# Kernel tuning notes

Hardware: AMD Instinct MI355X
Metric: run time of the kernel (lower is better)

The kernel has to match this reference:

```python
import jax, jax.numpy as jnp
import numpy as np

B, N, DIM = 4, 2048, 512
HEADS, DIM_HEAD = 8, 64
INNER = HEADS * DIM_HEAD  # == DIM, so to_out is Identity
LN_EPS = 1e-5
MASK_FILL = 1e-8  # faithful to torch.where(mask, attn, 1e-08)


def setup_inputs() -> dict:
    key = jax.random.key(0)
    k1, k2 = jax.random.split(key)
    x = jax.random.normal(k1, (B, N, DIM), dtype=jnp.float32)
    gamma = jnp.ones((DIM,), dtype=jnp.float32)
    beta = jnp.zeros((DIM,), dtype=jnp.float32)
    w_qkv = jax.random.normal(k2, (3 * INNER, DIM), dtype=jnp.float32) * (DIM ** -0.5)
    mask = jnp.tril(jnp.ones((N, N), dtype=bool))  # causal boolean mask, asserted 2-D in source
    return {"x": x, "gamma": gamma, "beta": beta, "w_qkv": w_qkv, "mask": mask}


def reference(x, gamma, beta, w_qkv, mask):
    # LayerNorm over last dim
    mu = jnp.mean(x, axis=-1, keepdims=True)
    var = jnp.var(x, axis=-1, keepdims=True)
    h = (x - mu) * jax.lax.rsqrt(var + LN_EPS) * gamma + beta
    # qkv projection (no bias), chunk into q, k, v
    qkv = h @ w_qkv.T  # [B, N, 3*INNER]
    q, k, v = jnp.split(qkv, 3, axis=-1)

    def to_heads(t):  # b n (h d) -> b h n d
        return t.reshape(B, N, HEADS, DIM_HEAD).transpose(0, 2, 1, 3)

    q, k, v = to_heads(q), to_heads(k), to_heads(v)
    # NOTE: original forward does NOT apply self.scale
    attn = jnp.einsum('bhnd,bhmd->bhnm', q, k)
    attn = jnp.where(mask[None, None, :, :], attn, MASK_FILL)
    p = jax.nn.softmax(attn, axis=-1)
    out = jnp.einsum('bhnm,bhmd->bhnd', p, v)
    out = out.transpose(0, 2, 1, 3).reshape(B, N, INNER)  # b h n d -> b n (h d)
    return out  # to_out is Identity since INNER == DIM
```

## Files before the change

kernel.cpp:

```cpp
#include <hip/hip_runtime.h>
#include <hip/hip_bf16.h>
#include <math.h>

#define B_  4
#define N_  2048
#define DIM_ 512
#define HEADS_ 8
#define QKV_ 1536
#define MASK_C 1e-8f
#define M_FIX 12.0f
#define LOG2E 1.44269504f

typedef __bf16 bf16_t;
typedef bf16_t bf16x8 __attribute__((ext_vector_type(8)));
typedef float  f32x4  __attribute__((ext_vector_type(4)));

__device__ __forceinline__ bf16_t f2b(float x) { return (bf16_t)x; }
__device__ __forceinline__ float  b2f(bf16_t x) { return (float)x; }

__device__ __forceinline__ f32x4 mfma16(bf16x8 a, bf16x8 b, f32x4 c) {
    return __builtin_amdgcn_mfma_f32_16x16x32_bf16(a, b, c, 0, 0, 0);
}

__device__ __forceinline__ void gload16(const bf16_t* g, bf16_t* l) {
    __builtin_amdgcn_global_load_lds(
        (const __attribute__((address_space(1))) unsigned int*)g,
        (__attribute__((address_space(3))) unsigned int*)l, 16, 0, 0);
}

__global__ __launch_bounds__(256) void ln_wsplit_kernel(const float* __restrict__ x,
                                                        const float* __restrict__ gamma,
                                                        const float* __restrict__ beta,
                                                        bf16_t* __restrict__ hh,
                                                        bf16_t* __restrict__ hl,
                                                        const float* __restrict__ wq,
                                                        bf16_t* __restrict__ wh,
                                                        bf16_t* __restrict__ wl) {
    int blk = blockIdx.x;
    int t = threadIdx.x;
    if (blk >= B_ * N_) {
        int i = ((blk - B_ * N_) * 256 + t) * 4;
        float4 v = *(const float4*)&wq[i];
        float vv[4] = {v.x, v.y, v.z, v.w};
        #pragma unroll
        for (int j = 0; j < 4; j++) {
            bf16_t hi = f2b(vv[j]);
            wh[i + j] = hi;
            wl[i + j] = f2b(vv[j] - b2f(hi));
        }
        return;
    }
    int row = blk;
    const float* xr = x + (size_t)row * DIM_;
    float e0 = xr[t];
    float e1 = xr[t + 256];
    float s  = e0 + e1;
    float sq = e0 * e0 + e1 * e1;
    for (int off = 32; off; off >>= 1) {
        s  += __shfl_xor(s, off);
        sq += __shfl_xor(sq, off);
    }
    __shared__ float red[8];
    int w = t >> 6;
    if ((t & 63) == 0) { red[w] = s; red[4 + w] = sq; }
    __syncthreads();
    float S  = red[0] + red[1] + red[2] + red[3];
    float SQ = red[4] + red[5] + red[6] + red[7];
    float mu = S * (1.0f / DIM_);
    float var = SQ * (1.0f / DIM_) - mu * mu;
    float rs = rsqrtf(var + 1e-5f);
    float y0 = (e0 - mu) * rs * gamma[t] + beta[t];
    float y1 = (e1 - mu) * rs * gamma[t + 256] + beta[t + 256];
    size_t base = (size_t)row * DIM_;
    bf16_t h0 = f2b(y0), h1 = f2b(y1);
    hh[base + t] = h0;       hl[base + t] = f2b(y0 - b2f(h0));
    hh[base + t + 256] = h1; hl[base + t + 256] = f2b(y1 - b2f(h1));
}

__global__ __launch_bounds__(256, 3) void qkv_gemm(const bf16_t* __restrict__ hh,
                                                   const bf16_t* __restrict__ hl,
                                                   const bf16_t* __restrict__ wh,
                                                   const bf16_t* __restrict__ wl,
                                                   bf16_t* __restrict__ qh, bf16_t* __restrict__ ql,
                                                   bf16_t* __restrict__ kh, bf16_t* __restrict__ kl,
                                                   bf16_t* __restrict__ vth,
                                                   float* __restrict__ part) {
    __shared__ __align__(16) bf16_t smem[16896];
    bf16_t* Ah = smem;
    bf16_t* Al = smem + 4096;
    bf16_t* Bh = smem + 8192;
    bf16_t* Bl = smem + 12288;
    int bm = blockIdx.x & 63;
    int bn = blockIdx.x >> 6;
    int t = threadIdx.x;
    int w = t >> 6, lane = t & 63, quad = lane >> 4, l16 = lane & 15;

    f32x4 acc[2][8];
    #pragma unroll
    for (int i = 0; i < 2; i++)
        #pragma unroll
        for (int j = 0; j < 8; j++) acc[i][j] = (f32x4)(0.0f);

    int sl = lane & 15, sg = lane >> 4;
    size_t gA0 = (size_t)(bm * 128 + w * 32 + sl) * 512 + sg * 8;
    size_t gB0 = (size_t)(bn * 128 + w * 32 + sl) * 512 + sg * 8;

    for (int k0 = 0; k0 < 512; k0 += 32) {
        __syncthreads();
        #pragma unroll
        for (int c = 0; c < 2; c++) {
            size_t ga = gA0 + k0 + (size_t)c * 16 * 512;
            size_t gb = gB0 + k0 + (size_t)c * 16 * 512;
            int lo = w * 1024 + c * 512;
            gload16(&hh[ga], Ah + lo);
            gload16(&hl[ga], Al + lo);
            gload16(&wh[gb], Bh + lo);
            gload16(&wl[gb], Bl + lo);
        }
        __syncthreads();

        bf16x8 aH[2], aL[2];
        #pragma unroll
        for (int mt = 0; mt < 2; mt++) {
            int ab = (w * 2 + mt) * 512 + quad * 128 + l16 * 8;
            aH[mt] = *(const bf16x8*)&Ah[ab];
            aL[mt] = *(const bf16x8*)&Al[ab];
        }
        #pragma unroll
        for (int nt = 0; nt < 8; nt++) {
            int bb = nt * 512 + quad * 128 + l16 * 8;
            bf16x8 bH = *(const bf16x8*)&Bh[bb];
            bf16x8 bL = *(const bf16x8*)&Bl[bb];
            #pragma unroll
            for (int mt = 0; mt < 2; mt++) {
                acc[mt][nt] = mfma16(aH[mt], bH, acc[mt][nt]);
                acc[mt][nt] = mfma16(aH[mt], bL, acc[mt][nt]);
                acc[mt][nt] = mfma16(aL[mt], bH, acc[mt][nt]);
            }
        }
    }

    if (bn < 8) {
        #pragma unroll
        for (int mt = 0; mt < 2; mt++)
            #pragma unroll
            for (int nt = 0; nt < 8; nt++)
                #pragma unroll
                for (int reg = 0; reg < 4; reg++) {
                    float v = acc[mt][nt][reg];
                    int row = bm * 128 + w * 32 + mt * 16 + quad * 4 + reg;
                    int n = bn * 128 + nt * 16 + l16;
                    bf16_t hi = f2b(v);
                    bf16_t lo = f2b(v - b2f(hi));
                    if (n < 512) {
                        size_t a = (size_t)row * 512 + n;
                        qh[a] = hi; ql[a] = lo;
                    } else {
                        size_t a = (size_t)row * 512 + (n - 512);
                        kh[a] = hi; kl[a] = lo;
                    }
                }
    } else {
        int bb = bm >> 4, key0 = (bm & 15) * 128;
        int n = t & 127, mc = (t >> 7) * 64;
        int head = (bn - 8) * 2 + (n >> 6), dd = n & 63;
        size_t obase = ((size_t)((bb * 8 + head) * 64 + dd)) * 2048 + key0 + mc;
        float Ssum = 0.0f;
        #pragma unroll
        for (int pass = 0; pass < 2; pass++) {
            __syncthreads();
            #pragma unroll
            for (int mt = 0; mt < 2; mt++)
                #pragma unroll
                for (int nt = 0; nt < 8; nt++)
                    #pragma unroll
                    for (int reg = 0; reg < 4; reg++) {
                        float v = acc[mt][nt][reg];
                        bf16_t hi = f2b(v);
                        bf16_t val = pass ? f2b(v - b2f(hi)) : hi;
                        smem[(w * 32 + mt * 16 + quad * 4 + reg) * 132 + nt * 16 + l16] = val;
                    }
            __syncthreads();
            #pragma unroll
            for (int i = 0; i < 64; i += 8) {
                __align__(16) bf16_t v8[8];
                #pragma unroll
                for (int j = 0; j < 8; j++) {
                    v8[j] = smem[(mc + i + j) * 132 + n];
                    Ssum += b2f(v8[j]);
                }
                if (pass == 0)
                    *(uint4*)&vth[obase + i] = *(const uint4*)v8;
            }
        }
        int tt = (key0 >> 6) + (mc >> 6);
        part[((size_t)((bb * 8 + head) * 32 + tt)) * 64 + dd] = Ssum;
    }
}

__global__ __launch_bounds__(256, 4) void attn_kernel(const bf16_t* __restrict__ qh,
                                                      const bf16_t* __restrict__ ql,
                                                      const bf16_t* __restrict__ kh,
                                                      const bf16_t* __restrict__ kl,
                                                      const bf16_t* __restrict__ vth,
                                                      const float* __restrict__ part,
                                                      float* __restrict__ out) {
    __shared__ __align__(16) bf16_t smem[17152];
    __shared__ float sufl[4][64];
    char* lds = (char*)smem;
    bf16_t* Ps = smem + 12288;

    int blk = blockIdx.x;
    int bh = blk & 31;
    int gi = blk >> 5;
    int g3 = gi & 7;
    int q4 = gi >> 3;
    int rt;
    if (q4 == 0)      rt = 31 - g3;
    else if (q4 == 1) rt = g3;
    else if (q4 == 2) rt = 23 - g3;
    else              rt = 8 + g3;
    int b = bh >> 3, head = bh & 7;
    int t = threadIdx.x;
    int w = t >> 6, lane = t & 63, quad = lane >> 4, l16 = lane & 15;

    {
        int d = t & 63, g = t >> 6;
        float s = 0.0f;
        for (int tt = rt + 1 + g; tt < 32; tt += 4)
            s += part[((size_t)bh * 32 + tt) * 64 + d];
        sufl[g][d] = s;
    }

    bf16x8 qAH[2], qAL[2];
    {
        int qrow = rt * 64 + w * 16 + l16;
        size_t g = ((size_t)(b * N_ + qrow)) * 512 + head * 64 + quad * 8;
        qAH[0] = *(const bf16x8*)&qh[g];
        qAH[1] = *(const bf16x8*)&qh[g + 32];
        qAL[0] = *(const bf16x8*)&ql[g];
        qAL[1] = *(const bf16x8*)&ql[g + 32];
    }
    bf16x8 ones;
    #pragma unroll
    for (int j = 0; j < 8; j++) ones[j] = f2b(1.0f);

    f32x4 O[4];
    #pragma unroll
    for (int nt = 0; nt < 4; nt++) O[nt] = (f32x4)(0.0f);
    f32x4 Lacc = (f32x4)(0.0f);
    const float mbias = M_FIX * LOG2E;

    int r = t >> 2, c16 = t & 3;
    int swz = (r & 7) << 4;
    int lk0 = r * 128 + ((c16 * 32)      ^ swz);
    int lk1 = r * 128 + ((c16 * 32 + 16) ^ swz);
    size_t gk = ((size_t)(b * N_ + r)) * 512 + head * 64 + c16 * 16;
    size_t gv = ((size_t)(bh * 64 + r)) * 2048 + c16 * 16;

    uint4 pKh0 = *(const uint4*)&kh[gk];
    uint4 pKh1 = *(const uint4*)&kh[gk + 8];
    uint4 pKl0 = *(const uint4*)&kl[gk];
    uint4 pKl1 = *(const uint4*)&kl[gk + 8];
    uint4 pVh0 = *(const uint4*)&vth[gv];
    uint4 pVh1 = *(const uint4*)&vth[gv + 8];

    for (int jt = 0; jt <= rt; jt++) {
        __syncthreads();
        *(uint4*)(lds + lk0)         = pKh0;
        *(uint4*)(lds + lk1)         = pKh1;
        *(uint4*)(lds + 8192 + lk0)  = pKl0;
        *(uint4*)(lds + 8192 + lk1)  = pKl1;
        *(uint4*)(lds + 16384 + lk0) = pVh0;
        *(uint4*)(lds + 16384 + lk1) = pVh1;
        __syncthreads();

        if (jt < rt) {
            gk += (size_t)64 * 512;
            gv += 64;
            pKh0 = *(const uint4*)&kh[gk];
            pKh1 = *(const uint4*)&kh[gk + 8];
            pKl0 = *(const uint4*)&kl[gk];
            pKl1 = *(const uint4*)&kl[gk + 8];
            pVh0 = *(const uint4*)&vth[gv];
            pVh1 = *(const uint4*)&vth[gv + 8];
        }

        f32x4 S[4];
        #pragma unroll
        for (int nt = 0; nt < 4; nt++) S[nt] = (f32x4)(0.0f);
        __builtin_amdgcn_s_setprio(1);
        #pragma unroll
        for (int khf = 0; khf < 2; khf++) {
            #pragma unroll
            for (int nt = 0; nt < 4; nt++) {
                int row = nt * 16 + l16;
                int bc = (khf * 64 + quad * 16) ^ ((row & 7) << 4);
                bf16x8 bH = *(const bf16x8*)(lds + row * 128 + bc);
                bf16x8 bL = *(const bf16x8*)(lds + 8192 + row * 128 + bc);
                S[nt] = mfma16(qAH[khf], bH, S[nt]);
                S[nt] = mfma16(qAH[khf], bL, S[nt]);
                S[nt] = mfma16(qAL[khf], bH, S[nt]);
            }
        }
        __builtin_amdgcn_s_setprio(0);

        if (jt == rt) {
            int lrow = w * 16 + quad * 4;
            #pragma unroll
            for (int nt = 0; nt < 4; nt++)
                #pragma unroll
                for (int reg = 0; reg < 4; reg++)
                    if (nt * 16 + l16 > lrow + reg) S[nt][reg] = MASK_C;
        }

        #pragma unroll
        for (int nt = 0; nt < 4; nt++)
            #pragma unroll
            for (int reg = 0; reg < 4; reg++)
                Ps[(w * 16 + quad * 4 + reg) * 76 + nt * 16 + l16] =
                    f2b(exp2f(fmaf(S[nt][reg], LOG2E, -mbias)));

        bf16x8 pH[2];
        #pragma unroll
        for (int khf = 0; khf < 2; khf++)
            pH[khf] = *(const bf16x8*)&Ps[(w * 16 + l16) * 76 + khf * 32 + quad * 8];

        __builtin_amdgcn_s_setprio(1);
        #pragma unroll
        for (int khf = 0; khf < 2; khf++) Lacc = mfma16(pH[khf], ones, Lacc);

        #pragma unroll
        for (int khf = 0; khf < 2; khf++) {
            #pragma unroll
            for (int nt = 0; nt < 4; nt++) {
                int row = nt * 16 + l16;
                int bc = (khf * 64 + quad * 16) ^ ((row & 7) << 4);
                bf16x8 vB = *(const bf16x8*)(lds + 16384 + row * 128 + bc);
                O[nt] = mfma16(pH[khf], vB, O[nt]);
            }
        }
        __builtin_amdgcn_s_setprio(0);
    }

    float L[4];
    #pragma unroll
    for (int reg = 0; reg < 4; reg++) L[reg] = Lacc[reg];
    int cnt = N_ - (rt + 1) * 64;
    if (cnt > 0) {
        float pc = expf(MASK_C - M_FIX);
        float sv[4];
        #pragma unroll
        for (int nt = 0; nt < 4; nt++) {
            int d = nt * 16 + l16;
            sv[nt] = sufl[0][d] + sufl[1][d] + sufl[2][d] + sufl[3][d];
        }
        #pragma unroll
        for (int reg = 0; reg < 4; reg++) {
            L[reg] += pc * (float)cnt;
            #pragma unroll
            for (int nt = 0; nt < 4; nt++) O[nt][reg] += pc * sv[nt];
        }
    }

    #pragma unroll
    for (int reg = 0; reg < 4; reg++) {
        float rl = 1.0f / L[reg];
        int row = rt * 64 + w * 16 + quad * 4 + reg;
        #pragma unroll
        for (int nt = 0; nt < 4; nt++)
            out[((size_t)(b * N_ + row)) * DIM_ + head * 64 + nt * 16 + l16] =
                O[nt][reg] * rl;
    }
}

extern "C" void kernel_launch(void* const* d_in, const int* in_sizes, int n_in,
                              void* d_out, int out_size, void* d_ws, size_t ws_size,
                              hipStream_t stream) {
    const float* x     = (const float*)d_in[0];
    const float* gamma = (const float*)d_in[1];
    const float* beta  = (const float*)d_in[2];
    const float* w_qkv = (const float*)d_in[3];
    float* out = (float*)d_out;

    const size_t HW = (size_t)8192 * 512;
    const size_t WN = (size_t)1536 * 512;
    bf16_t* hh  = (bf16_t*)d_ws;
    bf16_t* hl  = hh + HW;
    bf16_t* qh  = hl + HW;
    bf16_t* ql  = qh + HW;
    bf16_t* kh  = ql + HW;
    bf16_t* kl  = kh + HW;
    bf16_t* vth = kl + HW;
    bf16_t* vtl = vth + HW;
    bf16_t* wh  = vtl + HW;
    bf16_t* wl  = wh + WN;
    float*  part = (float*)(wl + WN);

    ln_wsplit_kernel<<<B_ * N_ + 768, 256, 0, stream>>>(x, gamma, beta, hh, hl,
                                                        w_qkv, wh, wl);
    qkv_gemm<<<768, 256, 0, stream>>>(hh, hl, wh, wl, qh, ql, kh, kl, vth, part);
    attn_kernel<<<1024, 256, 0, stream>>>(qh, ql, kh, kl, vth, part, out);
}
```

Before: 207.1 us.

## Stage QKV GEMM through registers and read attention K/V directly from global

The QKV GEMM replaces direct global-to-LDS loads with register-prefetched tiles written into a padded (stride 40) LDS layout, overlapping the next k-slice fetch with compute. The attention kernel drops LDS staging of K/V entirely and has each wave load its MFMA operands straight from global memory (relying on L1/L2), removing two block barriers per tile. This trades sync and LDS traffic for redundant global loads across the four waves and exposed load latency without explicit prefetch.

```diff
diff --git a/kernel.cpp b/kernel.cpp
--- a/kernel.cpp
+++ b/kernel.cpp
@@ -20,12 +20,6 @@
 
 __device__ __forceinline__ f32x4 mfma16(bf16x8 a, bf16x8 b, f32x4 c) {
     return __builtin_amdgcn_mfma_f32_16x16x32_bf16(a, b, c, 0, 0, 0);
-}
-
-__device__ __forceinline__ void gload16(const bf16_t* g, bf16_t* l) {
-    __builtin_amdgcn_global_load_lds(
-        (const __attribute__((address_space(1))) unsigned int*)g,
-        (__attribute__((address_space(3))) unsigned int*)l, 16, 0, 0);
 }
 
 __global__ __launch_bounds__(256) void ln_wsplit_kernel(const float* __restrict__ x,
@@ -85,11 +79,11 @@
                                                    bf16_t* __restrict__ kh, bf16_t* __restrict__ kl,
                                                    bf16_t* __restrict__ vth,
                                                    float* __restrict__ part) {
-    __shared__ __align__(16) bf16_t smem[16896];
+    __shared__ __align__(16) bf16_t smem[20480];
     bf16_t* Ah = smem;
-    bf16_t* Al = smem + 4096;
-    bf16_t* Bh = smem + 8192;
-    bf16_t* Bl = smem + 12288;
+    bf16_t* Al = smem + 5120;
+    bf16_t* Bh = smem + 10240;
+    bf16_t* Bl = smem + 15360;
     int bm = blockIdx.x & 63;
     int bn = blockIdx.x >> 6;
     int t = threadIdx.x;
@@ -101,36 +95,53 @@
         #pragma unroll
         for (int j = 0; j < 8; j++) acc[i][j] = (f32x4)(0.0f);
 
-    int sl = lane & 15, sg = lane >> 4;
-    size_t gA0 = (size_t)(bm * 128 + w * 32 + sl) * 512 + sg * 8;
-    size_t gB0 = (size_t)(bn * 128 + w * 32 + sl) * 512 + sg * 8;
+    int sr = t >> 1, skc = (t & 1) * 16;
+    size_t gA = (size_t)(bm * 128 + sr) * 512 + skc;
+    size_t gB = (size_t)(bn * 128 + sr) * 512 + skc;
+
+    uint4 rAh0 = *(const uint4*)&hh[gA];
+    uint4 rAh1 = *(const uint4*)&hh[gA + 8];
+    uint4 rAl0 = *(const uint4*)&hl[gA];
+    uint4 rAl1 = *(const uint4*)&hl[gA + 8];
+    uint4 rBh0 = *(const uint4*)&wh[gB];
+    uint4 rBh1 = *(const uint4*)&wh[gB + 8];
+    uint4 rBl0 = *(const uint4*)&wl[gB];
+    uint4 rBl1 = *(const uint4*)&wl[gB + 8];
 
     for (int k0 = 0; k0 < 512; k0 += 32) {
         __syncthreads();
-        #pragma unroll
-        for (int c = 0; c < 2; c++) {
-            size_t ga = gA0 + k0 + (size_t)c * 16 * 512;
-            size_t gb = gB0 + k0 + (size_t)c * 16 * 512;
-            int lo = w * 1024 + c * 512;
-            gload16(&hh[ga], Ah + lo);
-            gload16(&hl[ga], Al + lo);
-            gload16(&wh[gb], Bh + lo);
-            gload16(&wl[gb], Bl + lo);
-        }
+        *(uint4*)&Ah[sr * 40 + skc]     = rAh0;
+        *(uint4*)&Ah[sr * 40 + skc + 8] = rAh1;
+        *(uint4*)&Al[sr * 40 + skc]     = rAl0;
+        *(uint4*)&Al[sr * 40 + skc + 8] = rAl1;
+        *(uint4*)&Bh[sr * 40 + skc]     = rBh0;
+        *(uint4*)&Bh[sr * 40 + skc + 8] = rBh1;
+        *(uint4*)&Bl[sr * 40 + skc]     = rBl0;
+        *(uint4*)&Bl[sr * 40 + skc + 8] = rBl1;
         __syncthreads();
 
+        if (k0 < 480) {
+            int kn = k0 + 32;
+            rAh0 = *(const uint4*)&hh[gA + kn];
+            rAh1 = *(const uint4*)&hh[gA + kn + 8];
+            rAl0 = *(const uint4*)&hl[gA + kn];
+            rAl1 = *(const uint4*)&hl[gA + kn + 8];
+            rBh0 = *(const uint4*)&wh[gB + kn];
+            rBh1 = *(const uint4*)&wh[gB + kn + 8];
+            rBl0 = *(const uint4*)&wl[gB + kn];
+            rBl1 = *(const uint4*)&wl[gB + kn + 8];
+        }
+
         bf16x8 aH[2], aL[2];
         #pragma unroll
         for (int mt = 0; mt < 2; mt++) {
-            int ab = (w * 2 + mt) * 512 + quad * 128 + l16 * 8;
-            aH[mt] = *(const bf16x8*)&Ah[ab];
-            aL[mt] = *(const bf16x8*)&Al[ab];
+            aH[mt] = *(const bf16x8*)&Ah[(w * 32 + mt * 16 + l16) * 40 + quad * 8];
+            aL[mt] = *(const bf16x8*)&Al[(w * 32 + mt * 16 + l16) * 40 + quad * 8];
         }
         #pragma unroll
         for (int nt = 0; nt < 8; nt++) {
-            int bb = nt * 512 + quad * 128 + l16 * 8;
-            bf16x8 bH = *(const bf16x8*)&Bh[bb];
-            bf16x8 bL = *(const bf16x8*)&Bl[bb];
+            bf16x8 bH = *(const bf16x8*)&Bh[(nt * 16 + l16) * 40 + quad * 8];
+            bf16x8 bL = *(const bf16x8*)&Bl[(nt * 16 + l16) * 40 + quad * 8];
             #pragma unroll
             for (int mt = 0; mt < 2; mt++) {
                 acc[mt][nt] = mfma16(aH[mt], bH, acc[mt][nt]);
@@ -205,10 +216,8 @@
                                                       const bf16_t* __restrict__ vth,
                                                       const float* __restrict__ part,
                                                       float* __restrict__ out) {
-    __shared__ __align__(16) bf16_t smem[17152];
+    __shared__ __align__(16) bf16_t Ps[4][16][76];
     __shared__ float sufl[4][64];
-    char* lds = (char*)smem;
-    bf16_t* Ps = smem + 12288;
 
     int blk = blockIdx.x;
     int bh = blk & 31;
@@ -225,11 +234,11 @@
     int w = t >> 6, lane = t & 63, quad = lane >> 4, l16 = lane & 15;
 
     {
-        int d = t & 63, g = t >> 6;
+        int d = t & 63;
         float s = 0.0f;
-        for (int tt = rt + 1 + g; tt < 32; tt += 4)
+        for (int tt = rt + 1 + w; tt < 32; tt += 4)
             s += part[((size_t)bh * 32 + tt) * 64 + d];
-        sufl[g][d] = s;
+        sufl[w][d] = s;
     }
 
     bf16x8 qAH[2], qAL[2];
@@ -251,40 +260,12 @@
     f32x4 Lacc = (f32x4)(0.0f);
     const float mbias = M_FIX * LOG2E;
 
-    int r = t >> 2, c16 = t & 3;
-    int swz = (r & 7) << 4;
-    int lk0 = r * 128 + ((c16 * 32)      ^ swz);
-    int lk1 = r * 128 + ((c16 * 32 + 16) ^ swz);
-    size_t gk = ((size_t)(b * N_ + r)) * 512 + head * 64 + c16 * 16;
-    size_t gv = ((size_t)(bh * 64 + r)) * 2048 + c16 * 16;
-
-    uint4 pKh0 = *(const uint4*)&kh[gk];
-    uint4 pKh1 = *(const uint4*)&kh[gk + 8];
-    uint4 pKl0 = *(const uint4*)&kl[gk];
-    uint4 pKl1 = *(const uint4*)&kl[gk + 8];
-    uint4 pVh0 = *(const uint4*)&vth[gv];
-    uint4 pVh1 = *(const uint4*)&vth[gv + 8];
+    const bf16_t* kHb = kh + ((size_t)(b * N_ + l16)) * 512 + head * 64 + quad * 8;
+    const bf16_t* kLb = kl + ((size_t)(b * N_ + l16)) * 512 + head * 64 + quad * 8;
+    const bf16_t* vBb = vth + ((size_t)(bh * 64 + l16)) * 2048 + quad * 8;
 
     for (int jt = 0; jt <= rt; jt++) {
-        __syncthreads();
-        *(uint4*)(lds + lk0)         = pKh0;
-        *(uint4*)(lds + lk1)         = pKh1;
-        *(uint4*)(lds + 8192 + lk0)  = pKl0;
-        *(uint4*)(lds + 8192 + lk1)  = pKl1;
-        *(uint4*)(lds + 16384 + lk0) = pVh0;
-        *(uint4*)(lds + 16384 + lk1) = pVh1;
-        __syncthreads();
-
-        if (jt < rt) {
-            gk += (size_t)64 * 512;
-            gv += 64;
-            pKh0 = *(const uint4*)&kh[gk];
-            pKh1 = *(const uint4*)&kh[gk + 8];
-            pKl0 = *(const uint4*)&kl[gk];
-            pKl1 = *(const uint4*)&kl[gk + 8];
-            pVh0 = *(const uint4*)&vth[gv];
-            pVh1 = *(const uint4*)&vth[gv + 8];
-        }
+        size_t krow = (size_t)jt * 64 * 512;
 
         f32x4 S[4];
         #pragma unroll
@@ -294,10 +275,9 @@
         for (int khf = 0; khf < 2; khf++) {
             #pragma unroll
             for (int nt = 0; nt < 4; nt++) {
-                int row = nt * 16 + l16;
-                int bc = (khf * 64 + quad * 16) ^ ((row & 7) << 4);
-                bf16x8 bH = *(const bf16x8*)(lds + row * 128 + bc);
-                bf16x8 bL = *(const bf16x8*)(lds + 8192 + row * 128 + bc);
+                size_t a = krow + (size_t)(nt * 16) * 512 + khf * 32;
+                bf16x8 bH = *(const bf16x8*)(kHb + a);
+                bf16x8 bL = *(const bf16x8*)(kLb + a);
                 S[nt] = mfma16(qAH[khf], bH, S[nt]);
                 S[nt] = mfma16(qAH[khf], bL, S[nt]);
                 S[nt] = mfma16(qAL[khf], bH, S[nt]);
@@ -305,6 +285,14 @@
         }
         __builtin_amdgcn_s_setprio(0);
 
+        bf16x8 vB[2][4];
+        #pragma unroll
+        for (int khf = 0; khf < 2; khf++)
+            #pragma unroll
+            for (int nt = 0; nt < 4; nt++)
+                vB[khf][nt] = *(const bf16x8*)(vBb + (size_t)(nt * 16) * 2048 +
+                                               jt * 64 + khf * 32);
+
         if (jt == rt) {
             int lrow = w * 16 + quad * 4;
             #pragma unroll
@@ -318,30 +306,27 @@
         for (int nt = 0; nt < 4; nt++)
             #pragma unroll
             for (int reg = 0; reg < 4; reg++)
-                Ps[(w * 16 + quad * 4 + reg) * 76 + nt * 16 + l16] =
+                Ps[w][quad * 4 + reg][nt * 16 + l16] =
                     f2b(exp2f(fmaf(S[nt][reg], LOG2E, -mbias)));
 
         bf16x8 pH[2];
         #pragma unroll
         for (int khf = 0; khf < 2; khf++)
-            pH[khf] = *(const bf16x8*)&Ps[(w * 16 + l16) * 76 + khf * 32 + quad * 8];
+            pH[khf] = *(const bf16x8*)&Ps[w][l16][khf * 32 + quad * 8];
 
         __builtin_amdgcn_s_setprio(1);
         #pragma unroll
         for (int khf = 0; khf < 2; khf++) Lacc = mfma16(pH[khf], ones, Lacc);
 
         #pragma unroll
-        for (int khf = 0; khf < 2; khf++) {
-            #pragma unroll
-            for (int nt = 0; nt < 4; nt++) {
-                int row = nt * 16 + l16;
-                int bc = (khf * 64 + quad * 16) ^ ((row & 7) << 4);
-                bf16x8 vB = *(const bf16x8*)(lds + 16384 + row * 128 + bc);
-                O[nt] = mfma16(pH[khf], vB, O[nt]);
-            }
-        }
+        for (int khf = 0; khf < 2; khf++)
+            #pragma unroll
+            for (int nt = 0; nt < 4; nt++)
+                O[nt] = mfma16(pH[khf], vB[khf][nt], O[nt]);
         __builtin_amdgcn_s_setprio(0);
     }
+
+    __syncthreads();
 
     float L[4];
     #pragma unroll
```

New measurement: 309.3 us. 49.3% more time.

## Register-prefetch QKV GEMM tiles into padded LDS instead of direct global-to-LDS loads

Applied to the files above, without the earlier changes.

The QKV GEMM stops using global_load_lds for its tiles. It now prefetches the next K-slice into registers while the current slice computes, then writes it to an LDS layout padded to a row stride of 40 to avoid bank conflicts. The LayerNorm kernel switches to float2 loads and packed 4-byte bf16 stores. The aim is to overlap global latency with MFMA work, at the cost of more VGPRs and LDS, which may lower occupancy under launch_bounds(256,3).

```diff
diff --git a/kernel.cpp b/kernel.cpp
--- a/kernel.cpp
+++ b/kernel.cpp
@@ -20,12 +20,6 @@
 
 __device__ __forceinline__ f32x4 mfma16(bf16x8 a, bf16x8 b, f32x4 c) {
     return __builtin_amdgcn_mfma_f32_16x16x32_bf16(a, b, c, 0, 0, 0);
-}
-
-__device__ __forceinline__ void gload16(const bf16_t* g, bf16_t* l) {
-    __builtin_amdgcn_global_load_lds(
-        (const __attribute__((address_space(1))) unsigned int*)g,
-        (__attribute__((address_space(3))) unsigned int*)l, 16, 0, 0);
 }
 
 __global__ __launch_bounds__(256) void ln_wsplit_kernel(const float* __restrict__ x,
@@ -52,8 +46,8 @@
     }
     int row = blk;
     const float* xr = x + (size_t)row * DIM_;
-    float e0 = xr[t];
-    float e1 = xr[t + 256];
+    float2 xv = *(const float2*)&xr[2 * t];
+    float e0 = xv.x, e1 = xv.y;
     float s  = e0 + e1;
     float sq = e0 * e0 + e1 * e1;
     for (int off = 32; off; off >>= 1) {
@@ -69,12 +63,16 @@
     float mu = S * (1.0f / DIM_);
     float var = SQ * (1.0f / DIM_) - mu * mu;
     float rs = rsqrtf(var + 1e-5f);
-    float y0 = (e0 - mu) * rs * gamma[t] + beta[t];
-    float y1 = (e1 - mu) * rs * gamma[t + 256] + beta[t + 256];
-    size_t base = (size_t)row * DIM_;
+    float2 gv = *(const float2*)&gamma[2 * t];
+    float2 bv = *(const float2*)&beta[2 * t];
+    float y0 = (e0 - mu) * rs * gv.x + bv.x;
+    float y1 = (e1 - mu) * rs * gv.y + bv.y;
+    size_t base = (size_t)row * DIM_ + 2 * t;
     bf16_t h0 = f2b(y0), h1 = f2b(y1);
-    hh[base + t] = h0;       hl[base + t] = f2b(y0 - b2f(h0));
-    hh[base + t + 256] = h1; hl[base + t + 256] = f2b(y1 - b2f(h1));
+    __align__(4) bf16_t hp[2] = {h0, h1};
+    __align__(4) bf16_t lp[2] = {f2b(y0 - b2f(h0)), f2b(y1 - b2f(h1))};
+    *(unsigned int*)&hh[base] = *(unsigned int*)hp;
+    *(unsigned int*)&hl[base] = *(unsigned int*)lp;
 }
 
 __global__ __launch_bounds__(256, 3) void qkv_gemm(const bf16_t* __restrict__ hh,
@@ -85,11 +83,11 @@
                                                    bf16_t* __restrict__ kh, bf16_t* __restrict__ kl,
                                                    bf16_t* __restrict__ vth,
                                                    float* __restrict__ part) {
-    __shared__ __align__(16) bf16_t smem[16896];
+    __shared__ __align__(16) bf16_t smem[20480];
     bf16_t* Ah = smem;
-    bf16_t* Al = smem + 4096;
-    bf16_t* Bh = smem + 8192;
-    bf16_t* Bl = smem + 12288;
+    bf16_t* Al = smem + 5120;
+    bf16_t* Bh = smem + 10240;
+    bf16_t* Bl = smem + 15360;
     int bm = blockIdx.x & 63;
     int bn = blockIdx.x >> 6;
     int t = threadIdx.x;
@@ -101,36 +99,53 @@
         #pragma unroll
         for (int j = 0; j < 8; j++) acc[i][j] = (f32x4)(0.0f);
 
-    int sl = lane & 15, sg = lane >> 4;
-    size_t gA0 = (size_t)(bm * 128 + w * 32 + sl) * 512 + sg * 8;
-    size_t gB0 = (size_t)(bn * 128 + w * 32 + sl) * 512 + sg * 8;
+    int sr = t >> 1, skc = (t & 1) * 16;
+    size_t gA = (size_t)(bm * 128 + sr) * 512 + skc;
+    size_t gB = (size_t)(bn * 128 + sr) * 512 + skc;
+
+    uint4 rAh0 = *(const uint4*)&hh[gA];
+    uint4 rAh1 = *(const uint4*)&hh[gA + 8];
+    uint4 rAl0 = *(const uint4*)&hl[gA];
+    uint4 rAl1 = *(const uint4*)&hl[gA + 8];
+    uint4 rBh0 = *(const uint4*)&wh[gB];
+    uint4 rBh1 = *(const uint4*)&wh[gB + 8];
+    uint4 rBl0 = *(const uint4*)&wl[gB];
+    uint4 rBl1 = *(const uint4*)&wl[gB + 8];
 
     for (int k0 = 0; k0 < 512; k0 += 32) {
         __syncthreads();
-        #pragma unroll
-        for (int c = 0; c < 2; c++) {
-            size_t ga = gA0 + k0 + (size_t)c * 16 * 512;
-            size_t gb = gB0 + k0 + (size_t)c * 16 * 512;
-            int lo = w * 1024 + c * 512;
-            gload16(&hh[ga], Ah + lo);
-            gload16(&hl[ga], Al + lo);
-            gload16(&wh[gb], Bh + lo);
-            gload16(&wl[gb], Bl + lo);
-        }
+        *(uint4*)&Ah[sr * 40 + skc]     = rAh0;
+        *(uint4*)&Ah[sr * 40 + skc + 8] = rAh1;
+        *(uint4*)&Al[sr * 40 + skc]     = rAl0;
+        *(uint4*)&Al[sr * 40 + skc + 8] = rAl1;
+        *(uint4*)&Bh[sr * 40 + skc]     = rBh0;
+        *(uint4*)&Bh[sr * 40 + skc + 8] = rBh1;
+        *(uint4*)&Bl[sr * 40 + skc]     = rBl0;
+        *(uint4*)&Bl[sr * 40 + skc + 8] = rBl1;
         __syncthreads();
 
+        if (k0 < 480) {
+            int kn = k0 + 32;
+            rAh0 = *(const uint4*)&hh[gA + kn];
+            rAh1 = *(const uint4*)&hh[gA + kn + 8];
+            rAl0 = *(const uint4*)&hl[gA + kn];
+            rAl1 = *(const uint4*)&hl[gA + kn + 8];
+            rBh0 = *(const uint4*)&wh[gB + kn];
+            rBh1 = *(const uint4*)&wh[gB + kn + 8];
+            rBl0 = *(const uint4*)&wl[gB + kn];
+            rBl1 = *(const uint4*)&wl[gB + kn + 8];
+        }
+
         bf16x8 aH[2], aL[2];
         #pragma unroll
         for (int mt = 0; mt < 2; mt++) {
-            int ab = (w * 2 + mt) * 512 + quad * 128 + l16 * 8;
-            aH[mt] = *(const bf16x8*)&Ah[ab];
-            aL[mt] = *(const bf16x8*)&Al[ab];
+            aH[mt] = *(const bf16x8*)&Ah[(w * 32 + mt * 16 + l16) * 40 + quad * 8];
+            aL[mt] = *(const bf16x8*)&Al[(w * 32 + mt * 16 + l16) * 40 + quad * 8];
         }
         #pragma unroll
         for (int nt = 0; nt < 8; nt++) {
-            int bb = nt * 512 + quad * 128 + l16 * 8;
-            bf16x8 bH = *(const bf16x8*)&Bh[bb];
-            bf16x8 bL = *(const bf16x8*)&Bl[bb];
+            bf16x8 bH = *(const bf16x8*)&Bh[(nt * 16 + l16) * 40 + quad * 8];
+            bf16x8 bL = *(const bf16x8*)&Bl[(nt * 16 + l16) * 40 + quad * 8];
             #pragma unroll
             for (int mt = 0; mt < 2; mt++) {
                 acc[mt][nt] = mfma16(aH[mt], bH, acc[mt][nt]);
```

New measurement: 193.3 us. -6.7%, faster.
